# Kernel optimization log

Measured on AMD Instinct MI355X. Metric: run time of the kernel, lower is better.

## Reference

```python
import jax, jax.numpy as jnp
import numpy as np

N_NODES = 100000
N_EDGES = 1600000
IN_DIM = 128
HID = 128
OUT_DIM = 10
N_CONV = 4
N_GRAPHS = 128


def setup_inputs() -> dict:
    key = jax.random.key(0)
    ks = jax.random.split(key, 12)
    x = jax.random.normal(ks[0], (N_NODES, IN_DIM), dtype=jnp.float32)
    edge_index = jax.random.randint(ks[1], (2, N_EDGES), 0, N_NODES, dtype=jnp.int64)
    batch = jnp.sort(jax.random.randint(ks[2], (N_NODES,), 0, N_GRAPHS, dtype=jnp.int64))
    s = 1.0 / np.sqrt(HID)
    enc_W = jax.random.uniform(ks[3], (IN_DIM, HID), jnp.float32, -s, s)
    enc_b = jax.random.uniform(ks[4], (HID,), jnp.float32, -s, s)
    conv_W = jax.random.uniform(ks[5], (N_CONV, HID, HID), jnp.float32, -s, s)
    conv_b = jax.random.uniform(ks[6], (N_CONV, HID), jnp.float32, -s, s)
    dec_W = jax.random.uniform(ks[7], (HID, OUT_DIM), jnp.float32, -s, s)
    dec_b = jax.random.uniform(ks[8], (OUT_DIM,), jnp.float32, -s, s)
    return {"x": x, "enc_W": enc_W, "enc_b": enc_b, "conv_W": conv_W,
            "conv_b": conv_b, "dec_W": dec_W, "dec_b": dec_b,
            "edge_index": edge_index, "batch": batch}


def reference(x, enc_W, enc_b, conv_W, conv_b, dec_W, dec_b, edge_index, batch):
    N = x.shape[0]
    # encode MLP
    h = jax.nn.relu(x @ enc_W + enc_b)
    # GCN normalization with self-loops (PyG GCNConv default):
    # norm_e = deg(col)^-1/2 * deg(row)^-1/2 over A + I
    loops = jnp.arange(N, dtype=edge_index.dtype)
    row = jnp.concatenate([edge_index[0], loops])  # source j
    col = jnp.concatenate([edge_index[1], loops])  # target i
    deg = jax.ops.segment_sum(jnp.ones_like(col, dtype=h.dtype), col, num_segments=N)
    dinv = jnp.where(deg > 0, jax.lax.rsqrt(deg), 0.0)
    norm = dinv[row] * dinv[col]  # [E+N]
    for l in range(conv_W.shape[0]):
        m = h @ conv_W[l]                      # [N, HID] linear first
        msg = m[row] * norm[:, None]           # [E+N, HID] gather + scale
        agg = jax.ops.segment_sum(msg, col, num_segments=N)  # scatter-add
        h = jax.nn.relu(agg + conv_b[l])
    # global_add_pool over graph ids
    g = jax.ops.segment_sum(h, batch, num_segments=N_GRAPHS)  # [G, HID]
    return g @ dec_W + dec_b
```

## Files before the change

### kernel.cpp

```cpp
#include <hip/hip_runtime.h>

#define NN 100000
#define NE 1600000
#define HID 128
#define OUT_DIM 10
#define N_CONV 4
#define N_GRAPHS 128

#define NBUCK 196
#define CCHUNK 4096
#define NCB ((NE + CCHUNK - 1) / CCHUNK)


__global__ __launch_bounds__(256) void k_zero(float* __restrict__ g,
                                              int* __restrict__ coarse_cnt) {
  int i = blockIdx.x * 256 + threadIdx.x;
  if (i < N_GRAPHS * HID) g[i] = 0.0f;
  if (i < NBUCK + 1) coarse_cnt[i] = 0;
}


__global__ __launch_bounds__(256) void k_hist(const int* __restrict__ ecol,
                                              int* __restrict__ coarse_cnt) {
  __shared__ int cnt[NBUCK];
  for (int i = threadIdx.x; i < NBUCK; i += 256) cnt[i] = 0;
  __syncthreads();
  int base = blockIdx.x * CCHUNK;
#pragma unroll
  for (int i = 0; i < 16; ++i) {
    int e = base + i * 256 + threadIdx.x;
    if (e < NE) atomicAdd(&cnt[ecol[e] >> 9], 1);
  }
  __syncthreads();
  for (int i = threadIdx.x; i < NBUCK; i += 256)
    if (cnt[i]) atomicAdd(&coarse_cnt[i], cnt[i]);
}


__global__ __launch_bounds__(256) void k_scanb(const int* __restrict__ coarse_cnt,
                                               int* __restrict__ bucket_base,
                                               int* __restrict__ bcur,
                                               int* __restrict__ row_ptr) {
  __shared__ int s[256];
  int t = threadIdx.x;
  int v = (t < NBUCK) ? coarse_cnt[t] : 0;
  s[t] = v;
  __syncthreads();
  for (int off = 1; off < 256; off <<= 1) {
    int u = (t >= off) ? s[t - off] : 0;
    __syncthreads();
    s[t] += u;
    __syncthreads();
  }
  if (t < NBUCK) {
    int excl = s[t] - v;
    bucket_base[t] = excl;
    bcur[t] = excl;
  }
  if (t == 0) { bucket_base[NBUCK] = NE; row_ptr[NN] = NE; }
}


__global__ __launch_bounds__(256) void k_scatter(const int* __restrict__ erow,
                                                 const int* __restrict__ ecol,
                                                 int* __restrict__ bcur,
                                                 int* __restrict__ edge_buf) {
  __shared__ int rs[CCHUNK];
  __shared__ unsigned char rb[CCHUNK];
  __shared__ int cnt[NBUCK + 1];
  __shared__ int lbase[NBUCK + 1];
  __shared__ int lcur[NBUCK + 1];
  __shared__ int grun[NBUCK];
  __shared__ int sscan[256];
  __shared__ int sTotal;

  const int t = threadIdx.x;
  const int base = blockIdx.x * CCHUNK;

  for (int i = t; i < NBUCK + 1; i += 256) cnt[i] = 0;
  __syncthreads();

  int myb[16];
#pragma unroll
  for (int i = 0; i < 16; ++i) {
    int e = base + i * 256 + t;
    int b = NBUCK;
    if (e < NE) b = ecol[e] >> 9;
    myb[i] = b;
    if (b < NBUCK) atomicAdd(&cnt[b], 1);
  }
  __syncthreads();

  int cv = (t < NBUCK) ? cnt[t] : 0;
  sscan[t] = cv;
  __syncthreads();
  for (int off = 1; off < 256; off <<= 1) {
    int u = (t >= off) ? sscan[t - off] : 0;
    __syncthreads();
    sscan[t] += u;
    __syncthreads();
  }
  if (t < NBUCK) {
    int excl = sscan[t] - cv;
    lbase[t] = excl;
    lcur[t] = excl;
    if (cv > 0) grun[t] = atomicAdd(&bcur[t], cv);
  }
  if (t == 255) sTotal = sscan[255];
  __syncthreads();

#pragma unroll
  for (int i = 0; i < 16; ++i) {
    int b = myb[i];
    if (b < NBUCK) {
      int e = base + i * 256 + t;
      int packed = erow[e] | ((ecol[e] & 511) << 17);
      int pos = atomicAdd(&lcur[b], 1);
      rs[pos] = packed;
      rb[pos] = (unsigned char)b;
    }
  }
  __syncthreads();

  int total = sTotal;
  for (int pos = t; pos < total; pos += 256) {
    int b = rb[pos];
    edge_buf[grun[b] + (pos - lbase[b])] = rs[pos];
  }
}


__global__ __launch_bounds__(512) void k_build(const int* __restrict__ bucket_base,
                                               const int* __restrict__ edge_buf,
                                               int* __restrict__ row_ptr,
                                               float* __restrict__ dinv,
                                               int* __restrict__ csr_src) {
  __shared__ int cnt[512];
  __shared__ int s[512];
  __shared__ int cur[512];
  const int b = blockIdx.x;
  const int t = threadIdx.x;
  const int r0 = bucket_base[b];
  const int r1 = bucket_base[b + 1];

  cnt[t] = 0;
  __syncthreads();
  for (int e = r0 + t; e < r1; e += 512) {
    int dl = ((unsigned)edge_buf[e]) >> 17;
    atomicAdd(&cnt[dl], 1);
  }
  __syncthreads();
  s[t] = cnt[t];
  __syncthreads();
  for (int off = 1; off < 512; off <<= 1) {
    int u = (t >= off) ? s[t - off] : 0;
    __syncthreads();
    s[t] += u;
    __syncthreads();
  }
  int node = b * 512 + t;
  int excl = s[t] - cnt[t];
  if (node < NN) {
    row_ptr[node] = r0 + excl;
    dinv[node] = rsqrtf((float)(cnt[t] + 1));
  }
  cur[t] = r0 + excl;
  __syncthreads();
  for (int e = r0 + t; e < r1; e += 512) {
    int v = edge_buf[e];
    int dl = ((unsigned)v) >> 17;
    int pos = atomicAdd(&cur[dl], 1);
    csr_src[pos] = v & 0x1FFFF;
  }
}


__global__ __launch_bounds__(256) void gemm128v2(const float* __restrict__ A,
                                                 const float* __restrict__ W,
                                                 float* __restrict__ out,
                                                 const float* __restrict__ bias,
                                                 int relu,
                                                 const float* __restrict__ rowscale,
                                                 int N) {
  __shared__ float sA[128][36];
  __shared__ float sW[32][132];
  const int tid = threadIdx.x;
  const int tr = tid >> 4;
  const int tc = tid & 15;
  const int rowBase = blockIdx.x * 128;

  float4 acc0[8], acc1[8];
#pragma unroll
  for (int r = 0; r < 8; ++r) {
    acc0[r] = make_float4(0.f, 0.f, 0.f, 0.f);
    acc1[r] = make_float4(0.f, 0.f, 0.f, 0.f);
  }

  for (int kc = 0; kc < 128; kc += 32) {
    {
      int r = tid >> 1;
      int half = tid & 1;
      int row = rowBase + r;
      const float* src = &A[(size_t)row * 128 + kc + half * 16];
#pragma unroll
      for (int j = 0; j < 4; ++j) {
        float4 v = make_float4(0.f, 0.f, 0.f, 0.f);
        if (row < N) v = *(const float4*)&src[j * 4];
        *(float4*)&sA[r][half * 16 + j * 4] = v;
      }
    }
    {
      int k = tid >> 3;
      int cg = (tid & 7) * 16;
      const float* src = &W[(size_t)(kc + k) * 128 + cg];
#pragma unroll
      for (int j = 0; j < 4; ++j) {
        *(float4*)&sW[k][cg + j * 4] = *(const float4*)&src[j * 4];
      }
    }
    __syncthreads();

#pragma unroll
    for (int kk = 0; kk < 32; kk += 4) {
      float4 b0[4], b1[4];
#pragma unroll
      for (int j = 0; j < 4; ++j) {
        b0[j] = *(float4*)&sW[kk + j][tc * 4];
        b1[j] = *(float4*)&sW[kk + j][tc * 4 + 64];
      }
#pragma unroll
      for (int r = 0; r < 8; ++r) {
        float4 a = *(float4*)&sA[tr + 16 * r][kk];
        acc0[r].x += a.x * b0[0].x; acc0[r].y += a.x * b0[0].y;
        acc0[r].z += a.x * b0[0].z; acc0[r].w += a.x * b0[0].w;
        acc1[r].x += a.x * b1[0].x; acc1[r].y += a.x * b1[0].y;
        acc1[r].z += a.x * b1[0].z; acc1[r].w += a.x * b1[0].w;

        acc0[r].x += a.y * b0[1].x; acc0[r].y += a.y * b0[1].y;
        acc0[r].z += a.y * b0[1].z; acc0[r].w += a.y * b0[1].w;
        acc1[r].x += a.y * b1[1].x; acc1[r].y += a.y * b1[1].y;
        acc1[r].z += a.y * b1[1].z; acc1[r].w += a.y * b1[1].w;

        acc0[r].x += a.z * b0[2].x; acc0[r].y += a.z * b0[2].y;
        acc0[r].z += a.z * b0[2].z; acc0[r].w += a.z * b0[2].w;
        acc1[r].x += a.z * b1[2].x; acc1[r].y += a.z * b1[2].y;
        acc1[r].z += a.z * b1[2].z; acc1[r].w += a.z * b1[2].w;

        acc0[r].x += a.w * b0[3].x; acc0[r].y += a.w * b0[3].y;
        acc0[r].z += a.w * b0[3].z; acc0[r].w += a.w * b0[3].w;
        acc1[r].x += a.w * b1[3].x; acc1[r].y += a.w * b1[3].y;
        acc1[r].z += a.w * b1[3].z; acc1[r].w += a.w * b1[3].w;
      }
    }
    __syncthreads();
  }

  float4 bv0 = make_float4(0.f, 0.f, 0.f, 0.f);
  float4 bv1 = make_float4(0.f, 0.f, 0.f, 0.f);
  if (bias) {
    bv0 = *(const float4*)&bias[tc * 4];
    bv1 = *(const float4*)&bias[tc * 4 + 64];
  }
#pragma unroll
  for (int r = 0; r < 8; ++r) {
    int row = rowBase + tr + 16 * r;
    if (row < N) {
      float sc = rowscale ? rowscale[row] : 1.0f;
      float4 v0, v1;
      v0.x = (acc0[r].x + bv0.x) * sc; v0.y = (acc0[r].y + bv0.y) * sc;
      v0.z = (acc0[r].z + bv0.z) * sc; v0.w = (acc0[r].w + bv0.w) * sc;
      v1.x = (acc1[r].x + bv1.x) * sc; v1.y = (acc1[r].y + bv1.y) * sc;
      v1.z = (acc1[r].z + bv1.z) * sc; v1.w = (acc1[r].w + bv1.w) * sc;
      if (relu) {
        v0.x = fmaxf(v0.x, 0.f); v0.y = fmaxf(v0.y, 0.f);
        v0.z = fmaxf(v0.z, 0.f); v0.w = fmaxf(v0.w, 0.f);
        v1.x = fmaxf(v1.x, 0.f); v1.y = fmaxf(v1.y, 0.f);
        v1.z = fmaxf(v1.z, 0.f); v1.w = fmaxf(v1.w, 0.f);
      }
      *(float4*)&out[(size_t)row * 128 + tc * 4] = v0;
      *(float4*)&out[(size_t)row * 128 + tc * 4 + 64] = v1;
    }
  }
}


__global__ __launch_bounds__(256) void gather_fused(const float* __restrict__ m,
                                                    const int* __restrict__ row_ptr,
                                                    const int* __restrict__ csr_src,
                                                    const float* __restrict__ dinv,
                                                    const float* __restrict__ bias,
                                                    float* __restrict__ h) {
  int t = blockIdx.x * 256 + threadIdx.x;
  int node = t >> 5;
  if (node >= NN) return;
  int lane = t & 31;

  float4 a0 = *(const float4*)&m[(size_t)node * 128 + lane * 4];
  float4 a1 = make_float4(0.f, 0.f, 0.f, 0.f);
  float4 a2 = make_float4(0.f, 0.f, 0.f, 0.f);
  float4 a3 = make_float4(0.f, 0.f, 0.f, 0.f);

  int beg = row_ptr[node];
  int end = row_ptr[node + 1];

  int k = beg;
  for (; k + 3 < end; k += 4) {
    int s0 = csr_src[k], s1 = csr_src[k + 1], s2 = csr_src[k + 2], s3 = csr_src[k + 3];
    float4 v0 = *(const float4*)&m[(size_t)s0 * 128 + lane * 4];
    float4 v1 = *(const float4*)&m[(size_t)s1 * 128 + lane * 4];
    float4 v2 = *(const float4*)&m[(size_t)s2 * 128 + lane * 4];
    float4 v3 = *(const float4*)&m[(size_t)s3 * 128 + lane * 4];
    a0.x += v0.x; a0.y += v0.y; a0.z += v0.z; a0.w += v0.w;
    a1.x += v1.x; a1.y += v1.y; a1.z += v1.z; a1.w += v1.w;
    a2.x += v2.x; a2.y += v2.y; a2.z += v2.z; a2.w += v2.w;
    a3.x += v3.x; a3.y += v3.y; a3.z += v3.z; a3.w += v3.w;
  }
  for (; k < end; ++k) {
    int s = csr_src[k];
    float4 v = *(const float4*)&m[(size_t)s * 128 + lane * 4];
    a0.x += v.x; a0.y += v.y; a0.z += v.z; a0.w += v.w;
  }
  a0.x += a1.x + a2.x + a3.x;
  a0.y += a1.y + a2.y + a3.y;
  a0.z += a1.z + a2.z + a3.z;
  a0.w += a1.w + a2.w + a3.w;

  float dn = dinv[node];
  float4 b = *(const float4*)&bias[lane * 4];
  float4 o;
  o.x = fmaxf(a0.x * dn + b.x, 0.f);
  o.y = fmaxf(a0.y * dn + b.y, 0.f);
  o.z = fmaxf(a0.z * dn + b.z, 0.f);
  o.w = fmaxf(a0.w * dn + b.w, 0.f);
  *(float4*)&h[(size_t)node * 128 + lane * 4] = o;
}


__global__ __launch_bounds__(128) void pool_kernel(const float* __restrict__ h,
                                                   const int* __restrict__ batch,
                                                   float* __restrict__ g) {
  int d = threadIdx.x;
  int chunk = (NN + gridDim.x - 1) / gridDim.x;
  int r0 = blockIdx.x * chunk;
  int r1 = min(NN, r0 + chunk);
  if (r0 >= r1) return;
  float acc = 0.f;
  int cur = batch[r0];
  for (int r = r0; r < r1; ++r) {
    int b = batch[r];
    if (b != cur) {
      atomicAdd(&g[(size_t)cur * HID + d], acc);
      acc = 0.f;
      cur = b;
    }
    acc += h[(size_t)r * HID + d];
  }
  atomicAdd(&g[(size_t)cur * HID + d], acc);
}


__global__ __launch_bounds__(256) void decode_kernel(const float* __restrict__ g,
                                                     const float* __restrict__ W,
                                                     const float* __restrict__ b,
                                                     float* __restrict__ out) {
  int idx = blockIdx.x * 256 + threadIdx.x;
  if (idx >= N_GRAPHS * OUT_DIM) return;
  int gi = idx / OUT_DIM;
  int o = idx % OUT_DIM;
  float acc = b[o];
#pragma unroll 8
  for (int k = 0; k < HID; ++k) acc += g[(size_t)gi * HID + k] * W[k * OUT_DIM + o];
  out[idx] = acc;
}


extern "C" void kernel_launch(void* const* d_in, const int* in_sizes, int n_in,
                              void* d_out, int out_size, void* d_ws, size_t ws_size,
                              hipStream_t stream) {
  const float* x      = (const float*)d_in[0];
  const float* enc_W  = (const float*)d_in[1];
  const float* enc_b  = (const float*)d_in[2];
  const float* conv_W = (const float*)d_in[3];
  const float* conv_b = (const float*)d_in[4];
  const float* dec_W  = (const float*)d_in[5];
  const float* dec_b  = (const float*)d_in[6];
  const int*   erow   = (const int*)d_in[7];
  const int*   ecol   = ((const int*)d_in[7]) + NE;
  const int*   batch  = (const int*)d_in[8];
  float* out = (float*)d_out;

  float* h          = (float*)d_ws;
  float* m          = h + (size_t)12800000;
  float* dinv       = m + (size_t)12800000;
  float* g          = dinv + 100352;
  int*   row_ptr    = (int*)(g + 16384);
  int*   csr_src    = row_ptr + 100352;
  int*   edge_buf   = csr_src + 1600000;
  int*   coarse_cnt = edge_buf + 1600000;
  int*   bucket_base= coarse_cnt + 256;
  int*   bcur       = bucket_base + 256;

  const int gemmBlocks = (NN + 127) / 128;
  const int nodeBlocks = (NN * 32 + 255) / 256;

  k_zero<<<64, 256, 0, stream>>>(g, coarse_cnt);
  k_hist<<<NCB, 256, 0, stream>>>(ecol, coarse_cnt);
  k_scanb<<<1, 256, 0, stream>>>(coarse_cnt, bucket_base, bcur, row_ptr);
  k_scatter<<<NCB, 256, 0, stream>>>(erow, ecol, bcur, edge_buf);
  k_build<<<NBUCK, 512, 0, stream>>>(bucket_base, edge_buf, row_ptr, dinv, csr_src);

  gemm128v2<<<gemmBlocks, 256, 0, stream>>>(x, enc_W, h, enc_b, 1, nullptr, NN);

  for (int l = 0; l < N_CONV; ++l) {
    const float* Wl = conv_W + (size_t)l * 128 * 128;
    const float* bl = conv_b + (size_t)l * 128;
    gemm128v2<<<gemmBlocks, 256, 0, stream>>>(h, Wl, m, nullptr, 0, dinv, NN);
    gather_fused<<<nodeBlocks, 256, 0, stream>>>(m, row_ptr, csr_src, dinv, bl, h);
  }

  pool_kernel<<<2048, 128, 0, stream>>>(h, batch, g);
  decode_kernel<<<(N_GRAPHS * OUT_DIM + 255) / 256, 256, 0, stream>>>(g, dec_W, dec_b, out);
}
```

Measured before the change: 935.6 us.

## Enlarge GEMM tile to 256 rows and use nontemporal loads/stores in gather

The dense GEMM now works on 256-row tiles. Each thread holds an 8x16 accumulator block instead of 8x8, which raises register-level reuse of the shared-memory A and W reads. The gather kernel reads CSR indices with nontemporal loads and writes h with nontemporal stores, to keep the gathered feature rows of m resident in cache. In exchange there are twice as many accumulator registers, so occupancy may drop, and only about 391 blocks exist to spread across the CUs.

After: 988.3 us. +5.6%, slower.

```diff
diff --git a/kernel.cpp b/kernel.cpp
--- a/kernel.cpp
+++ b/kernel.cpp
@@ -10,6 +10,8 @@
 #define NBUCK 196
 #define CCHUNK 4096
 #define NCB ((NE + CCHUNK - 1) / CCHUNK)
+
+typedef float nfloat4 __attribute__((ext_vector_type(4)));
 
 
 __global__ __launch_bounds__(256) void k_zero(float* __restrict__ g,
@@ -175,110 +177,97 @@
 }
 
 
-__global__ __launch_bounds__(256) void gemm128v2(const float* __restrict__ A,
-                                                 const float* __restrict__ W,
-                                                 float* __restrict__ out,
-                                                 const float* __restrict__ bias,
-                                                 int relu,
-                                                 const float* __restrict__ rowscale,
-                                                 int N) {
-  __shared__ float sA[128][36];
-  __shared__ float sW[32][132];
+__global__ __launch_bounds__(256, 2) void gemm256(const float* __restrict__ A,
+                                                  const float* __restrict__ W,
+                                                  float* __restrict__ out,
+                                                  const float* __restrict__ bias,
+                                                  int relu,
+                                                  const float* __restrict__ rowscale,
+                                                  int N) {
+  __shared__ float sA[256 * 36];
+  __shared__ float sW[32 * 132];
   const int tid = threadIdx.x;
-  const int tr = tid >> 4;
-  const int tc = tid & 15;
-  const int rowBase = blockIdx.x * 128;
-
-  float4 acc0[8], acc1[8];
-#pragma unroll
-  for (int r = 0; r < 8; ++r) {
-    acc0[r] = make_float4(0.f, 0.f, 0.f, 0.f);
-    acc1[r] = make_float4(0.f, 0.f, 0.f, 0.f);
-  }
+  const int rg = tid >> 3;
+  const int cg = tid & 7;
+  const int rowBase = blockIdx.x * 256;
+
+  float4 acc[8][4];
+#pragma unroll
+  for (int i = 0; i < 8; ++i)
+#pragma unroll
+    for (int q = 0; q < 4; ++q) acc[i][q] = make_float4(0.f, 0.f, 0.f, 0.f);
 
   for (int kc = 0; kc < 128; kc += 32) {
-    {
-      int r = tid >> 1;
-      int half = tid & 1;
-      int row = rowBase + r;
-      const float* src = &A[(size_t)row * 128 + kc + half * 16];
-#pragma unroll
-      for (int j = 0; j < 4; ++j) {
-        float4 v = make_float4(0.f, 0.f, 0.f, 0.f);
-        if (row < N) v = *(const float4*)&src[j * 4];
-        *(float4*)&sA[r][half * 16 + j * 4] = v;
-      }
+#pragma unroll
+    for (int rep = 0; rep < 8; ++rep) {
+      int rl = rep * 32 + (tid >> 3);
+      int row = rowBase + rl;
+      float4 v = make_float4(0.f, 0.f, 0.f, 0.f);
+      if (row < N) v = *(const float4*)&A[(size_t)row * 128 + kc + (tid & 7) * 4];
+      *(float4*)&sA[rl * 36 + (tid & 7) * 4] = v;
     }
     {
       int k = tid >> 3;
-      int cg = (tid & 7) * 16;
-      const float* src = &W[(size_t)(kc + k) * 128 + cg];
+      const float* src = &W[(size_t)(kc + k) * 128];
 #pragma unroll
       for (int j = 0; j < 4; ++j) {
-        *(float4*)&sW[k][cg + j * 4] = *(const float4*)&src[j * 4];
+        int f4 = (tid & 7) + 8 * j;
+        *(float4*)&sW[k * 132 + f4 * 4] = *(const float4*)&src[f4 * 4];
       }
     }
     __syncthreads();
 
 #pragma unroll
     for (int kk = 0; kk < 32; kk += 4) {
-      float4 b0[4], b1[4];
+      float4 a[8];
+#pragma unroll
+      for (int i = 0; i < 8; ++i)
+        a[i] = *(float4*)&sA[(rg + 32 * i) * 36 + kk];
 #pragma unroll
       for (int j = 0; j < 4; ++j) {
-        b0[j] = *(float4*)&sW[kk + j][tc * 4];
-        b1[j] = *(float4*)&sW[kk + j][tc * 4 + 64];
+        float4 b[4];
+#pragma unroll
+        for (int q = 0; q < 4; ++q)
+          b[q] = *(float4*)&sW[(kk + j) * 132 + (cg + 8 * q) * 4];
+#pragma unroll
+        for (int i = 0; i < 8; ++i) {
+          float av = (j == 0) ? a[i].x : (j == 1) ? a[i].y : (j == 2) ? a[i].z : a[i].w;
+#pragma unroll
+          for (int q = 0; q < 4; ++q) {
+            acc[i][q].x += av * b[q].x;
+            acc[i][q].y += av * b[q].y;
+            acc[i][q].z += av * b[q].z;
+            acc[i][q].w += av * b[q].w;
+          }
+        }
       }
-#pragma unroll
-      for (int r = 0; r < 8; ++r) {
-        float4 a = *(float4*)&sA[tr + 16 * r][kk];
-        acc0[r].x += a.x * b0[0].x; acc0[r].y += a.x * b0[0].y;
-        acc0[r].z += a.x * b0[0].z; acc0[r].w += a.x * b0[0].w;
-        acc1[r].x += a.x * b1[0].x; acc1[r].y += a.x * b1[0].y;
-        acc1[r].z += a.x * b1[0].z; acc1[r].w += a.x * b1[0].w;
-
-        acc0[r].x += a.y * b0[1].x; acc0[r].y += a.y * b0[1].y;
-        acc0[r].z += a.y * b0[1].z; acc0[r].w += a.y * b0[1].w;
-        acc1[r].x += a.y * b1[1].x; acc1[r].y += a.y * b1[1].y;
-        acc1[r].z += a.y * b1[1].z; acc1[r].w += a.y * b1[1].w;
-
-        acc0[r].x += a.z * b0[2].x; acc0[r].y += a.z * b0[2].y;
-        acc0[r].z += a.z * b0[2].z; acc0[r].w += a.z * b0[2].w;
-        acc1[r].x += a.z * b1[2].x; acc1[r].y += a.z * b1[2].y;
-        acc1[r].z += a.z * b1[2].z; acc1[r].w += a.z * b1[2].w;
-
-        acc0[r].x += a.w * b0[3].x; acc0[r].y += a.w * b0[3].y;
-        acc0[r].z += a.w * b0[3].z; acc0[r].w += a.w * b0[3].w;
-        acc1[r].x += a.w * b1[3].x; acc1[r].y += a.w * b1[3].y;
-        acc1[r].z += a.w * b1[3].z; acc1[r].w += a.w * b1[3].w;
-      }
-    }
-    __syncthreads();
-  }
-
-  float4 bv0 = make_float4(0.f, 0.f, 0.f, 0.f);
-  float4 bv1 = make_float4(0.f, 0.f, 0.f, 0.f);
-  if (bias) {
-    bv0 = *(const float4*)&bias[tc * 4];
-    bv1 = *(const float4*)&bias[tc * 4 + 64];
-  }
-#pragma unroll
-  for (int r = 0; r < 8; ++r) {
-    int row = rowBase + tr + 16 * r;
+    }
+    __syncthreads();
+  }
+
+  float4 bv[4];
+#pragma unroll
+  for (int q = 0; q < 4; ++q)
+    bv[q] = bias ? *(const float4*)&bias[(cg + 8 * q) * 4]
+                 : make_float4(0.f, 0.f, 0.f, 0.f);
+#pragma unroll
+  for (int i = 0; i < 8; ++i) {
+    int row = rowBase + rg + 32 * i;
     if (row < N) {
       float sc = rowscale ? rowscale[row] : 1.0f;
-      float4 v0, v1;
-      v0.x = (acc0[r].x + bv0.x) * sc; v0.y = (acc0[r].y + bv0.y) * sc;
-      v0.z = (acc0[r].z + bv0.z) * sc; v0.w = (acc0[r].w + bv0.w) * sc;
-      v1.x = (acc1[r].x + bv1.x) * sc; v1.y = (acc1[r].y + bv1.y) * sc;
-      v1.z = (acc1[r].z + bv1.z) * sc; v1.w = (acc1[r].w + bv1.w) * sc;
-      if (relu) {
-        v0.x = fmaxf(v0.x, 0.f); v0.y = fmaxf(v0.y, 0.f);
-        v0.z = fmaxf(v0.z, 0.f); v0.w = fmaxf(v0.w, 0.f);
-        v1.x = fmaxf(v1.x, 0.f); v1.y = fmaxf(v1.y, 0.f);
-        v1.z = fmaxf(v1.z, 0.f); v1.w = fmaxf(v1.w, 0.f);
+#pragma unroll
+      for (int q = 0; q < 4; ++q) {
+        float4 v;
+        v.x = (acc[i][q].x + bv[q].x) * sc;
+        v.y = (acc[i][q].y + bv[q].y) * sc;
+        v.z = (acc[i][q].z + bv[q].z) * sc;
+        v.w = (acc[i][q].w + bv[q].w) * sc;
+        if (relu) {
+          v.x = fmaxf(v.x, 0.f); v.y = fmaxf(v.y, 0.f);
+          v.z = fmaxf(v.z, 0.f); v.w = fmaxf(v.w, 0.f);
+        }
+        *(float4*)&out[(size_t)row * 128 + (cg + 8 * q) * 4] = v;
       }
-      *(float4*)&out[(size_t)row * 128 + tc * 4] = v0;
-      *(float4*)&out[(size_t)row * 128 + tc * 4 + 64] = v1;
     }
   }
 }
@@ -305,7 +294,10 @@
 
   int k = beg;
   for (; k + 3 < end; k += 4) {
-    int s0 = csr_src[k], s1 = csr_src[k + 1], s2 = csr_src[k + 2], s3 = csr_src[k + 3];
+    int s0 = __builtin_nontemporal_load(&csr_src[k]);
+    int s1 = __builtin_nontemporal_load(&csr_src[k + 1]);
+    int s2 = __builtin_nontemporal_load(&csr_src[k + 2]);
+    int s3 = __builtin_nontemporal_load(&csr_src[k + 3]);
     float4 v0 = *(const float4*)&m[(size_t)s0 * 128 + lane * 4];
     float4 v1 = *(const float4*)&m[(size_t)s1 * 128 + lane * 4];
     float4 v2 = *(const float4*)&m[(size_t)s2 * 128 + lane * 4];
@@ -316,7 +308,7 @@
     a3.x += v3.x; a3.y += v3.y; a3.z += v3.z; a3.w += v3.w;
   }
   for (; k < end; ++k) {
-    int s = csr_src[k];
+    int s = __builtin_nontemporal_load(&csr_src[k]);
     float4 v = *(const float4*)&m[(size_t)s * 128 + lane * 4];
     a0.x += v.x; a0.y += v.y; a0.z += v.z; a0.w += v.w;
   }
@@ -327,12 +319,12 @@
 
   float dn = dinv[node];
   float4 b = *(const float4*)&bias[lane * 4];
-  float4 o;
+  nfloat4 o;
   o.x = fmaxf(a0.x * dn + b.x, 0.f);
   o.y = fmaxf(a0.y * dn + b.y, 0.f);
   o.z = fmaxf(a0.z * dn + b.z, 0.f);
   o.w = fmaxf(a0.w * dn + b.w, 0.f);
-  *(float4*)&h[(size_t)node * 128 + lane * 4] = o;
+  __builtin_nontemporal_store(o, (nfloat4*)&h[(size_t)node * 128 + lane * 4]);
 }
 
 
@@ -400,7 +392,7 @@
   int*   bucket_base= coarse_cnt + 256;
   int*   bcur       = bucket_base + 256;
 
-  const int gemmBlocks = (NN + 127) / 128;
+  const int gemmBlocks = (NN + 255) / 256;
   const int nodeBlocks = (NN * 32 + 255) / 256;
 
   k_zero<<<64, 256, 0, stream>>>(g, coarse_cnt);
@@ -409,12 +401,12 @@
   k_scatter<<<NCB, 256, 0, stream>>>(erow, ecol, bcur, edge_buf);
   k_build<<<NBUCK, 512, 0, stream>>>(bucket_base, edge_buf, row_ptr, dinv, csr_src);
 
-  gemm128v2<<<gemmBlocks, 256, 0, stream>>>(x, enc_W, h, enc_b, 1, nullptr, NN);
+  gemm256<<<gemmBlocks, 256, 0, stream>>>(x, enc_W, h, enc_b, 1, nullptr, NN);
 
   for (int l = 0; l < N_CONV; ++l) {
     const float* Wl = conv_W + (size_t)l * 128 * 128;
     const float* bl = conv_b + (size_t)l * 128;
-    gemm128v2<<<gemmBlocks, 256, 0, stream>>>(h, Wl, m, nullptr, 0, dinv, NN);
+    gemm256<<<gemmBlocks, 256, 0, stream>>>(h, Wl, m, nullptr, 0, dinv, NN);
     gather_fused<<<nodeBlocks, 256, 0, stream>>>(m, row_ptr, csr_src, dinv, bl, h);
   }
 
```
